# Kernel tuning notes

Measured on AMD Instinct MI355X. Metric: run time of the kernel, lower is better.

The kernel has to match this reference:

```python
import jax, jax.numpy as jnp
import numpy as np

N_NODES = 50000
N_EDGES = 600000
D_FEAT = 128
N_CLASSES = 40


def setup_inputs() -> dict:
    key = jax.random.key(0)
    k1, k2, k3 = jax.random.split(key, 3)
    x = jax.random.normal(k1, (N_NODES, D_FEAT), dtype=jnp.float32)
    W = jax.random.normal(k2, (N_CLASSES, D_FEAT), dtype=jnp.float32) * (1.0 / np.sqrt(D_FEAT))
    b = jnp.zeros((N_CLASSES,), dtype=jnp.float32)
    edge_index = jax.random.randint(k3, (2, N_EDGES), 0, N_NODES, dtype=jnp.int64)
    return {"x": x, "W": W, "b": b, "edge_index": edge_index, "K": 2}


def reference(x, W, b, edge_index, K):
    n = x.shape[0]
    src, dst = edge_index[0], edge_index[1]
    # add self-loops (PyG gcn_norm, fill_value=1.0)
    loop = jnp.arange(n, dtype=edge_index.dtype)
    src_a = jnp.concatenate([src, loop])
    dst_a = jnp.concatenate([dst, loop])
    w = jnp.ones(src_a.shape[0], dtype=x.dtype)
    deg = jax.ops.segment_sum(w, dst_a, num_segments=n)
    dinv = jnp.where(deg > 0, jax.lax.rsqrt(deg), 0.0)
    norm = dinv[src_a] * dinv[dst_a]  # [E+N]
    h = x
    for _ in range(K):
        msg = norm[:, None] * h[src_a]           # [E+N, F] gather
        h = jax.ops.segment_sum(msg, dst_a, num_segments=n)  # scatter-add
    logits = h @ W.T + b
    return jax.nn.log_softmax(logits, axis=1)
```

## Files before the change

### kernel.cpp

```cpp
#include <hip/hip_runtime.h>
#include <math.h>

#define DFEAT 128
#define NC 40
#define YSTRIDE 64
#define NPART 8
#define CAP 48

__device__ __forceinline__ float bf2f(unsigned short u) {
    union { unsigned int i; float f; } c; c.i = ((unsigned int)u) << 16; return c.f;
}
__device__ __forceinline__ unsigned short f2bf(float f) {
    union { float f; unsigned int i; } c; c.f = f;
    unsigned int r = c.i + 0x7fff + ((c.i >> 16) & 1);
    return (unsigned short)(r >> 16);
}

__global__ __launch_bounds__(256) void zero_counts(int* __restrict__ counts, int n4) {
    int i = blockIdx.x * blockDim.x + threadIdx.x;
    int stride = gridDim.x * blockDim.x;
    int4* p = (int4*)counts;
    for (; i < n4; i += stride) p[i] = make_int4(0, 0, 0, 0);
}

__global__ __launch_bounds__(256) void fill_bucket(const int* __restrict__ src,
                                                   const int* __restrict__ dst, int e,
                                                   int n, int* __restrict__ counts,
                                                   int* __restrict__ bucket) {
    int part = blockIdx.x & (NPART - 1);
    int sub  = blockIdx.x >> 3;
    int slice = (n + NPART - 1) / NPART;
    int lo = part * slice, hi = min(n, lo + slice);
    int i = sub * blockDim.x + threadIdx.x;
    int stride = (gridDim.x >> 3) * blockDim.x;
    for (; i < e; i += stride) {
        int d = __builtin_nontemporal_load(&dst[i]);
        if (d < lo || d >= hi) continue;
        int s = __builtin_nontemporal_load(&src[i]);
        int pos = atomicAdd(&counts[d], 1);
        if (pos < CAP) bucket[(size_t)d * CAP + pos] = s;
    }
}

__global__ __launch_bounds__(256) void gemm_dinv(const float* __restrict__ x,
                                                 const float* __restrict__ W,
                                                 const int* __restrict__ counts,
                                                 int n, unsigned short* __restrict__ Y,
                                                 float* __restrict__ dinv) {
    __shared__ float Wl[NC * DFEAT];
    for (int i = threadIdx.x; i < NC * DFEAT; i += blockDim.x) Wl[i] = W[i];
    __syncthreads();
    int node = blockIdx.x * blockDim.x + threadIdx.x;
    if (node >= n) return;
    dinv[node] = rsqrtf((float)(counts[node] + 1));
    const float4* xr = (const float4*)(x + (size_t)node * DFEAT);
    float acc[NC];
    #pragma unroll
    for (int c = 0; c < NC; ++c) acc[c] = 0.0f;
    #pragma unroll 4
    for (int k4 = 0; k4 < DFEAT / 4; ++k4) {
        float4 xv = xr[k4];
        #pragma unroll
        for (int c = 0; c < NC; ++c) {
            float4 wv = *(const float4*)&Wl[c * DFEAT + k4 * 4];
            acc[c] = fmaf(xv.w, wv.w, fmaf(xv.z, wv.z,
                     fmaf(xv.y, wv.y, fmaf(xv.x, wv.x, acc[c]))));
        }
    }
    ushort4* yr = (ushort4*)(Y + (size_t)node * YSTRIDE);
    #pragma unroll
    for (int c4 = 0; c4 < 10; ++c4) {
        ushort4 o;
        o.x = f2bf(acc[4 * c4 + 0]); o.y = f2bf(acc[4 * c4 + 1]);
        o.z = f2bf(acc[4 * c4 + 2]); o.w = f2bf(acc[4 * c4 + 3]);
        yr[c4] = o;
    }
    #pragma unroll
    for (int c4 = 10; c4 < 16; ++c4) yr[c4] = make_ushort4(0, 0, 0, 0);
}


__device__ __forceinline__ void gather40(const unsigned short* __restrict__ Yin,
                                         const int* __restrict__ bucket,
                                         const float* __restrict__ dinv,
                                         float dv, int node, int deg, int lane,
                                         float acc[4]) {
    int q = lane >> 4, r = lane & 15;
    {
        ushort4 v = ((const ushort4*)Yin)[(size_t)node * 16 + r];
        float w = (q == 0) ? dv * dv : 0.0f;
        acc[0] += w * bf2f(v.x); acc[1] += w * bf2f(v.y);
        acc[2] += w * bf2f(v.z); acc[3] += w * bf2f(v.w);
    }
    const int* brow = bucket + (size_t)node * CAP;
    for (int base = 0; base < deg; base += 16) {
        int rem = deg - base;
        int sv = (lane < 16 && lane < rem) ? brow[base + lane] : 0;
        float dvv = dinv[__shfl(sv, lane & 15)];
        #pragma unroll
        for (int jj = 0; jj < 4; ++jj) {
            int el = jj * 4 + q;
            int sj = __shfl(sv, el);
            float wj = (el < rem) ? __shfl(dvv, el) * dv : 0.0f;
            ushort4 v = ((const ushort4*)Yin)[(size_t)sj * 16 + r];
            acc[0] += wj * bf2f(v.x); acc[1] += wj * bf2f(v.y);
            acc[2] += wj * bf2f(v.z); acc[3] += wj * bf2f(v.w);
        }
    }
    #pragma unroll
    for (int k = 0; k < 4; ++k) {
        acc[k] += __shfl_xor(acc[k], 16);
        acc[k] += __shfl_xor(acc[k], 32);
    }
}

__global__ void prop40(const unsigned short* __restrict__ Yin,
                       unsigned short* __restrict__ Yout,
                       const int* __restrict__ counts, const int* __restrict__ bucket,
                       const float* __restrict__ dinv, int n) {
    int node = (blockIdx.x * blockDim.x + threadIdx.x) >> 6;
    int lane = threadIdx.x & 63;
    if (node >= n) return;
    float dv = dinv[node];
    int deg = min(counts[node], CAP);
    float acc[4] = {0, 0, 0, 0};
    gather40(Yin, bucket, dinv, dv, node, deg, lane, acc);
    if ((lane >> 4) == 0) {
        ushort4 o;
        o.x = f2bf(acc[0]); o.y = f2bf(acc[1]); o.z = f2bf(acc[2]); o.w = f2bf(acc[3]);
        ((ushort4*)Yout)[(size_t)node * 16 + (lane & 15)] = o;
    }
}

__global__ void prop40_cls(const unsigned short* __restrict__ Yin,
                           const int* __restrict__ counts, const int* __restrict__ bucket,
                           const float* __restrict__ dinv, const float* __restrict__ bias,
                           float* __restrict__ out, int n) {
    int node = (blockIdx.x * blockDim.x + threadIdx.x) >> 6;
    int lane = threadIdx.x & 63;
    if (node >= n) return;
    float dv = dinv[node];
    int deg = min(counts[node], CAP);
    float acc[4] = {0, 0, 0, 0};
    gather40(Yin, bucket, dinv, dv, node, deg, lane, acc);
    int r = lane & 15;
    float v[4];
    float m = -INFINITY;
    #pragma unroll
    for (int k = 0; k < 4; ++k) {
        int c = 4 * r + k;
        if (c < NC) { v[k] = acc[k] + bias[c]; m = fmaxf(m, v[k]); }
        else v[k] = -INFINITY;
    }
    #pragma unroll
    for (int off = 1; off < 16; off <<= 1) m = fmaxf(m, __shfl_xor(m, off));
    float s = 0.0f;
    #pragma unroll
    for (int k = 0; k < 4; ++k) if (4 * r + k < NC) s += expf(v[k] - m);
    #pragma unroll
    for (int off = 1; off < 16; off <<= 1) s += __shfl_xor(s, off);
    float ls = logf(s) + m;
    if (lane < 10) {
        float4 o = make_float4(v[0] - ls, v[1] - ls, v[2] - ls, v[3] - ls);
        ((float4*)(out + (size_t)node * NC))[r] = o;
    }
}

extern "C" void kernel_launch(void* const* d_in, const int* in_sizes, int n_in,
                              void* d_out, int out_size, void* d_ws, size_t ws_size,
                              hipStream_t stream) {
    const float* x  = (const float*)d_in[0];
    const float* W  = (const float*)d_in[1];
    const float* b  = (const float*)d_in[2];
    const int*   ei = (const int*)d_in[3];

    int n  = in_sizes[0] / DFEAT;
    int e  = in_sizes[3] / 2;
    const int* src = ei;
    const int* dst = ei + e;

    char* ws = (char*)d_ws;
    size_t off = 0;
    auto alloc = [&](size_t bytes) -> void* {
        void* p = ws + off;
        off = (off + bytes + 255) & ~(size_t)255;
        return p;
    };
    unsigned short* Y0 = (unsigned short*)alloc((size_t)n * YSTRIDE * 2);
    unsigned short* Y1 = (unsigned short*)alloc((size_t)n * YSTRIDE * 2);
    float* dinv   = (float*)alloc((size_t)n * sizeof(float));
    int*   counts = (int*)  alloc(((size_t)n + 4) * sizeof(int));
    int*   bucket = (int*)  alloc((size_t)n * CAP * sizeof(int));

    int n4 = (n + 3) / 4;
    zero_counts<<<64, 256, 0, stream>>>(counts, n4);

    fill_bucket<<<1024, 256, 0, stream>>>(src, dst, e, n, counts, bucket);

    int gemmBlocks = (n + 255) / 256;
    gemm_dinv<<<gemmBlocks, 256, 0, stream>>>(x, W, counts, n, Y0, dinv);

    int waveBlocks = (n + 3) / 4;
    prop40<<<waveBlocks, 256, 0, stream>>>(Y0, Y1, counts, bucket, dinv, n);
    prop40_cls<<<waveBlocks, 256, 0, stream>>>(Y1, counts, bucket, dinv, b,
                                               (float*)d_out, n);
}
```

Before: 131.7 us.

## Shrink bf16 feature stride to 40 and partition prop blocks by node slice

Stores the projected bf16 features with a row stride of 40 instead of 64, so each gathered row touches 80 bytes rather than 128 and the zero-padding writes disappear. Only the first 10 lanes of each 16-lane group now load. The propagation kernels map blocks to node slices interleaved across 8 partitions, mirroring the fill_bucket partitioning, which may improve cache or XCD locality. Nontemporal loads in fill_bucket become plain loads and the zero kernel gets more blocks. Rows of 80 bytes are no longer 128-byte aligned, so a gathered row can span two cache lines.

```diff
diff --git a/kernel.cpp b/kernel.cpp
--- a/kernel.cpp
+++ b/kernel.cpp
@@ -3,7 +3,7 @@
 
 #define DFEAT 128
 #define NC 40
-#define YSTRIDE 64
+#define YSTRIDE 40
 #define NPART 8
 #define CAP 48
 
@@ -34,9 +34,9 @@
     int i = sub * blockDim.x + threadIdx.x;
     int stride = (gridDim.x >> 3) * blockDim.x;
     for (; i < e; i += stride) {
-        int d = __builtin_nontemporal_load(&dst[i]);
+        int d = dst[i];
         if (d < lo || d >= hi) continue;
-        int s = __builtin_nontemporal_load(&src[i]);
+        int s = src[i];
         int pos = atomicAdd(&counts[d], 1);
         if (pos < CAP) bucket[(size_t)d * CAP + pos] = s;
     }
@@ -75,8 +75,6 @@
         o.z = f2bf(acc[4 * c4 + 2]); o.w = f2bf(acc[4 * c4 + 3]);
         yr[c4] = o;
     }
-    #pragma unroll
-    for (int c4 = 10; c4 < 16; ++c4) yr[c4] = make_ushort4(0, 0, 0, 0);
 }
 
 
@@ -86,8 +84,10 @@
                                          float dv, int node, int deg, int lane,
                                          float acc[4]) {
     int q = lane >> 4, r = lane & 15;
+    bool act = (r < 10);
     {
-        ushort4 v = ((const ushort4*)Yin)[(size_t)node * 16 + r];
+        ushort4 v = act ? ((const ushort4*)(Yin + (size_t)node * YSTRIDE))[r]
+                        : make_ushort4(0, 0, 0, 0);
         float w = (q == 0) ? dv * dv : 0.0f;
         acc[0] += w * bf2f(v.x); acc[1] += w * bf2f(v.y);
         acc[2] += w * bf2f(v.z); acc[3] += w * bf2f(v.w);
@@ -102,7 +102,8 @@
             int el = jj * 4 + q;
             int sj = __shfl(sv, el);
             float wj = (el < rem) ? __shfl(dvv, el) * dv : 0.0f;
-            ushort4 v = ((const ushort4*)Yin)[(size_t)sj * 16 + r];
+            ushort4 v = act ? ((const ushort4*)(Yin + (size_t)sj * YSTRIDE))[r]
+                            : make_ushort4(0, 0, 0, 0);
             acc[0] += wj * bf2f(v.x); acc[1] += wj * bf2f(v.y);
             acc[2] += wj * bf2f(v.z); acc[3] += wj * bf2f(v.w);
         }
@@ -112,23 +113,34 @@
         acc[k] += __shfl_xor(acc[k], 16);
         acc[k] += __shfl_xor(acc[k], 32);
     }
+}
+
+__device__ __forceinline__ int part_node(int bid, int tid, int n, int* valid) {
+    int part = bid & (NPART - 1);
+    int sub  = bid >> 3;
+    int slice = (n + NPART - 1) / NPART;
+    int local = sub * 4 + (tid >> 6);
+    int node = part * slice + local;
+    *valid = (local < slice && node < n);
+    return node;
 }
 
 __global__ void prop40(const unsigned short* __restrict__ Yin,
                        unsigned short* __restrict__ Yout,
                        const int* __restrict__ counts, const int* __restrict__ bucket,
                        const float* __restrict__ dinv, int n) {
-    int node = (blockIdx.x * blockDim.x + threadIdx.x) >> 6;
+    int valid;
+    int node = part_node(blockIdx.x, threadIdx.x, n, &valid);
+    if (!valid) return;
     int lane = threadIdx.x & 63;
-    if (node >= n) return;
     float dv = dinv[node];
     int deg = min(counts[node], CAP);
     float acc[4] = {0, 0, 0, 0};
     gather40(Yin, bucket, dinv, dv, node, deg, lane, acc);
-    if ((lane >> 4) == 0) {
+    if (lane < 10) {
         ushort4 o;
         o.x = f2bf(acc[0]); o.y = f2bf(acc[1]); o.z = f2bf(acc[2]); o.w = f2bf(acc[3]);
-        ((ushort4*)Yout)[(size_t)node * 16 + (lane & 15)] = o;
+        ((ushort4*)(Yout + (size_t)node * YSTRIDE))[lane] = o;
     }
 }
 
@@ -136,9 +148,10 @@
                            const int* __restrict__ counts, const int* __restrict__ bucket,
                            const float* __restrict__ dinv, const float* __restrict__ bias,
                            float* __restrict__ out, int n) {
-    int node = (blockIdx.x * blockDim.x + threadIdx.x) >> 6;
+    int valid;
+    int node = part_node(blockIdx.x, threadIdx.x, n, &valid);
+    if (!valid) return;
     int lane = threadIdx.x & 63;
-    if (node >= n) return;
     float dv = dinv[node];
     int deg = min(counts[node], CAP);
     float acc[4] = {0, 0, 0, 0};
@@ -186,22 +199,23 @@
         off = (off + bytes + 255) & ~(size_t)255;
         return p;
     };
-    unsigned short* Y0 = (unsigned short*)alloc((size_t)n * YSTRIDE * 2);
-    unsigned short* Y1 = (unsigned short*)alloc((size_t)n * YSTRIDE * 2);
+    unsigned short* Y0 = (unsigned short*)alloc(((size_t)n * YSTRIDE + 16) * 2);
+    unsigned short* Y1 = (unsigned short*)alloc(((size_t)n * YSTRIDE + 16) * 2);
     float* dinv   = (float*)alloc((size_t)n * sizeof(float));
     int*   counts = (int*)  alloc(((size_t)n + 4) * sizeof(int));
     int*   bucket = (int*)  alloc((size_t)n * CAP * sizeof(int));
 
     int n4 = (n + 3) / 4;
-    zero_counts<<<64, 256, 0, stream>>>(counts, n4);
+    zero_counts<<<128, 256, 0, stream>>>(counts, n4);
 
     fill_bucket<<<1024, 256, 0, stream>>>(src, dst, e, n, counts, bucket);
 
     int gemmBlocks = (n + 255) / 256;
     gemm_dinv<<<gemmBlocks, 256, 0, stream>>>(x, W, counts, n, Y0, dinv);
 
-    int waveBlocks = (n + 3) / 4;
-    prop40<<<waveBlocks, 256, 0, stream>>>(Y0, Y1, counts, bucket, dinv, n);
-    prop40_cls<<<waveBlocks, 256, 0, stream>>>(Y1, counts, bucket, dinv, b,
+    int slice = (n + NPART - 1) / NPART;
+    int propBlocks = NPART * ((slice + 3) / 4);
+    prop40<<<propBlocks, 256, 0, stream>>>(Y0, Y1, counts, bucket, dinv, n);
+    prop40_cls<<<propBlocks, 256, 0, stream>>>(Y1, counts, bucket, dinv, b,
                                                (float*)d_out, n);
 }
```

Measured after the change: 131.8 us. About the same (+0.1%).
